# Kernel tuning notes

Measured on AMD Instinct MI355X. Metric: run time of the kernel, lower is better.

## Reference

```python
import jax, jax.numpy as jnp
import numpy as np

M_ANCH = 704   # 22 parts * 32 anchors
N_ANCH = 128   # object anchors


def reference(smpl_betas, object_rel_rotmat, object_rel_trans, object_anchors_org,
              v_template, shapedirs, J_regressor, pca_mean, pca_components,
              anchor_indices):
    b = smpl_betas.shape[0]
    v = v_template[None] + jnp.einsum('bk,vck->bvc', smpl_betas, shapedirs)   # [b,V,3]
    J = jnp.einsum('jv,bvc->bjc', J_regressor, v)                              # [b,55,3]
    v = v - J[:, :1]                                                           # root-center
    smpl_anchors = v[:, anchor_indices]                                        # [b,704,3]
    # --- encode: transform object anchors, broadcast offset diff, PCA ---
    obj_anchors = jnp.einsum('bnc,bdc->bnd', object_anchors_org, object_rel_rotmat) \
        + object_rel_trans[:, None, :]                                         # [b,128,3]
    offsets = obj_anchors[:, None, :, :] - smpl_anchors[:, :, None, :]         # [b,704,128,3]
    off_flat = offsets.reshape(b, -1)                                          # [b,270336]
    gamma = (off_flat - pca_mean[None]) @ pca_components.T                     # [b,128]
    # --- decode: PCA inverse ---
    off_rec = pca_mean[None] + gamma @ pca_components                          # [b,270336]
    # --- decode_object_RT: batched Procrustes via 3x3 SVD ---
    off4 = off_rec.reshape(b, M_ANCH, N_ANCH, 3)
    P = (smpl_anchors[:, :, None, :] + off4).reshape(b, -1, 3)                 # [b,m*n,3]
    Q = jnp.broadcast_to(object_anchors_org[:, None], (b, M_ANCH, N_ANCH, 3)).reshape(b, -1, 3)
    center_Q = Q.mean(axis=1, keepdims=True)
    Qc = Q - center_Q
    svd_mat = jnp.einsum('bic,bid->bcd', P, Qc)                                # P^T @ Qc, [b,3,3]
    u, s, vh = jnp.linalg.svd(svd_mat, full_matrices=False)
    d = jnp.linalg.det(u @ vh)                                                 # [b]
    dvec = jnp.concatenate([jnp.ones((b, 2), svd_mat.dtype), d[:, None]], axis=-1)
    R = (u * dvec[:, None, :]) @ vh                                            # u @ diag(1,1,d) @ vh
    T = (P - jnp.einsum('bij,bnj->bni', R, Q)).mean(axis=1)                    # [b,3]
    return gamma, R, T


def setup_inputs() -> dict:
    key = jax.random.key(0)
    ks = jax.random.split(key, 10)
    b, V, Jn, K = 64, 10475, 55, 10
    D = M_ANCH * N_ANCH * 3
    return {
        'smpl_betas': jax.random.normal(ks[0], (b, K), jnp.float32),
        'object_rel_rotmat': jax.random.normal(ks[1], (b, 3, 3), jnp.float32),
        'object_rel_trans': jax.random.normal(ks[2], (b, 3), jnp.float32),
        'object_anchors_org': jax.random.normal(ks[3], (b, N_ANCH, 3), jnp.float32),
        'v_template': jax.random.normal(ks[4], (V, 3), jnp.float32),
        'shapedirs': jax.random.normal(ks[5], (V, 3, K), jnp.float32) * 0.03,
        'J_regressor': jax.random.uniform(ks[6], (Jn, V), jnp.float32) / V,
        'pca_mean': jax.random.normal(ks[7], (D,), jnp.float32) * 0.1,
        'pca_components': jax.random.normal(ks[8], (128, D), jnp.float32) / np.sqrt(D),
        'anchor_indices': jax.random.randint(ks[9], (M_ANCH,), 0, V, jnp.int32),
    }
```

## Files before the change

### kernel.cpp

```cpp
#include <hip/hip_runtime.h>

#define V_CNT   10475
#define M_A     704
#define N_A     128
#define KB      10
#define D_TOT   270336
#define ROW384  384
#define NCHUNK  44
#define MT      16
#define LSTR    388

#define WS_JJ     0
#define WS_CMEAN  64
#define WS_MC     192
#define WS_V2C    576
#define WS_SASUM  960
#define WS_GWS    1152
#define WS_X      9344
#define WS_WP     169088
#define WS_UPART  488576
#define WS_TOTAL  2651264
#define WS_ZEROF  1152

#define NJ_BLK 28
#define NM_BLK 88
#define NP_BLK 64

__global__ __launch_bounds__(384) void k_pre(
    const float* __restrict__ Jr, const float* __restrict__ vt,
    const float* __restrict__ sd, const float* __restrict__ mean,
    const float* __restrict__ betas, const float* __restrict__ rot,
    const float* __restrict__ trans, const float* __restrict__ org,
    const int* __restrict__ anch,
    float* __restrict__ JJ, float* __restrict__ Mc,
    float* __restrict__ X, float* __restrict__ saSum) {
  __shared__ float orgL[384];
  __shared__ float red[384];
  __shared__ float small[24];
  const int blk = blockIdx.x, t = threadIdx.x;

  if (blk < NJ_BLK) {
    float acc[33];
#pragma unroll
    for (int i = 0; i < 33; ++i) acc[i] = 0.f;
    int v = blk * 384 + t;
    if (v < V_CNT) {
      float jr = Jr[v];
#pragma unroll
      for (int c = 0; c < 3; ++c) {
        acc[c] += jr * vt[v * 3 + c];
        const float* sp = sd + ((size_t)v * 3 + c) * KB;
#pragma unroll
        for (int k = 0; k < KB; ++k) acc[3 + c * KB + k] += jr * sp[k];
      }
    }
#pragma unroll
    for (int i = 0; i < 33; ++i) {
      float x = acc[i];
      for (int off = 32; off > 0; off >>= 1) x += __shfl_down(x, off);
      if ((t & 63) == 0) atomicAdd(&JJ[i], x);
    }
  } else if (blk < NJ_BLK + NM_BLK) {
    int j = blk - NJ_BLK;
    float a = 0.f;
#pragma unroll
    for (int mi = 0; mi < 8; ++mi)
      a += mean[(size_t)(j * 8 + mi) * ROW384 + t];
    atomicAdd(&Mc[t], a);
  } else {
    const int b = blk - (NJ_BLK + NM_BLK);
    if (t < 10) small[t] = betas[b * 10 + t];
    else if (t >= 10 && t < 19) small[t] = rot[b * 9 + (t - 10)];
    else if (t >= 19 && t < 22) small[t] = trans[b * 3 + (t - 19)];
    orgL[t] = org[(size_t)b * 384 + t];
    __syncthreads();
    {
      int n = t / 3, d = t % 3;
      X[(size_t)b * 2496 + t] =
          orgL[n * 3 + 0] * small[10 + d * 3 + 0] +
          orgL[n * 3 + 1] * small[10 + d * 3 + 1] +
          orgL[n * 3 + 2] * small[10 + d * 3 + 2] + small[19 + d];
    }
    float ps = 0.f;
    for (int e = t; e < 2112; e += 384) {
      int m = e / 3, c = e - m * 3;
      int a = anch[m];
      const float* sp = sd + ((size_t)a * 3 + c) * KB;
      float val = vt[a * 3 + c];
#pragma unroll
      for (int k = 0; k < KB; ++k) val += small[k] * sp[k];
      X[(size_t)b * 2496 + 384 + e] = val;
      ps += val;
    }
    red[t] = ps;
    __syncthreads();
    if (t < 3) {
      float s = 0.f;
#pragma unroll 8
      for (int j = 0; j < 128; ++j) s += red[t + 3 * j];
      saSum[b * 3 + t] = s;
    }
  }
}

__global__ __launch_bounds__(384) void k_pcpass(
    const float* __restrict__ pc, const float* __restrict__ mean,
    float* __restrict__ Upart, float* __restrict__ Wp,
    float* __restrict__ cmean) {
  __shared__ float tile[MT * LSTR];
  __shared__ float red[384];
  __shared__ float cred[6];
  const int t = threadIdx.x;
  const int pid = blockIdx.x & 127;
  const int chunk = blockIdx.x >> 7;
  const int m0 = chunk * MT;
  const float* row = pc + (size_t)pid * D_TOT + (size_t)m0 * ROW384;
  const float* mrow = mean + (size_t)m0 * ROW384;

  float cm = 0.f;
#pragma unroll
  for (int i = 0; i < 4; ++i) {
    int f = 1536 * i + 4 * t;
    float4 pv = *(const float4*)(row + f);
    float4 mv = *(const float4*)(mrow + f);
    cm += pv.x * mv.x + pv.y * mv.y + pv.z * mv.z + pv.w * mv.w;
    int m_l = 4 * i + t / 96;
    int col = (t % 96) * 4;
    *(float4*)(&tile[m_l * LSTR + col]) = pv;
  }
  __syncthreads();

  {
    float u = 0.f;
#pragma unroll
    for (int m = 0; m < MT; ++m) u += tile[m * LSTR + t];
    Upart[((size_t)chunk * 128 + pid) * 384 + t] = u;
  }
  {
    int grp = t / 48, mc = t % 48, m_l = mc / 3, c = mc % 3;
    const float* tp = &tile[m_l * LSTR + c];
    float vsp = 0.f;
#pragma unroll 8
    for (int j = 0; j < 16; ++j) vsp += tp[(grp * 16 + j) * 3];
    red[t] = vsp;
  }
  {
    float x = cm;
    for (int off = 32; off > 0; off >>= 1) x += __shfl_down(x, off);
    if ((t & 63) == 0) cred[t >> 6] = x;
  }
  __syncthreads();
  if (t < 48) {
    float vs = 0.f;
#pragma unroll
    for (int g = 0; g < 8; ++g) vs += red[g * 48 + t];
    Wp[(size_t)pid * 2496 + 384 + m0 * 3 + t] = -vs;
  }
  if (t == 0) {
    float s = cred[0] + cred[1] + cred[2] + cred[3] + cred[4] + cred[5];
    atomicAdd(&cmean[pid], s);
  }
}

__global__ __launch_bounds__(384) void k_red(
    const float* __restrict__ Upart, float* __restrict__ Wp,
    float* __restrict__ V2c) {
  __shared__ float red[384];
  const int pid = blockIdx.x, t = threadIdx.x;
  float u = 0.f;
#pragma unroll 4
  for (int c = 0; c < NCHUNK; ++c)
    u += Upart[((size_t)c * 128 + pid) * 384 + t];
  Wp[(size_t)pid * 2496 + t] = u;
  float s = 0.f;
  const float* vr = Wp + (size_t)pid * 2496 + 384;
#pragma unroll
  for (int j = 0; j < 6; ++j) {
    int idx = t + 384 * j;
    if (idx < 2112) s += vr[idx];
  }
  red[t] = s;
  __syncthreads();
  if (t < 3) {
    float acc = 0.f;
#pragma unroll 8
    for (int j = 0; j < 128; ++j) acc += red[t + 3 * j];
    V2c[t * 128 + pid] = -acc;
  }
}

__global__ __launch_bounds__(256) void k_gamma(
    const float* __restrict__ X, const float* __restrict__ Wp,
    float* __restrict__ gWS) {
  const int t = threadIdx.x;
  const int b = blockIdx.x >> 5, pg = blockIdx.x & 31;
  const int w = t >> 6, l = t & 63;
  const int p = pg * 4 + w;
  const float4* X4 = (const float4*)(X + (size_t)b * 2496);
  const float4* W4 = (const float4*)(Wp + (size_t)p * 2496);
  float s = 0.f;
#pragma unroll
  for (int i = 0; i < 10; ++i) {
    int idx = i * 64 + l;
    if (idx < 624) {
      float4 xv = X4[idx];
      float4 wv = W4[idx];
      s += xv.x * wv.x + xv.y * wv.y + xv.z * wv.z + xv.w * wv.w;
    }
  }
#pragma unroll
  for (int off = 32; off > 0; off >>= 1) s += __shfl_down(s, off);
  if (l == 0) gWS[b * 128 + p] = s;
}

__device__ inline double det3(const double A[3][3]) {
  return A[0][0] * (A[1][1] * A[2][2] - A[1][2] * A[2][1])
       - A[0][1] * (A[1][0] * A[2][2] - A[1][2] * A[2][0])
       + A[0][2] * (A[1][0] * A[2][1] - A[1][1] * A[2][0]);
}

__device__ void svd3_rotation(const float* S, float* Rout) {
  double M[3][3], B[3][3], Vv[3][3];
  for (int i = 0; i < 3; ++i)
    for (int j = 0; j < 3; ++j) M[i][j] = (double)S[i * 3 + j];
  for (int i = 0; i < 3; ++i)
    for (int j = 0; j < 3; ++j) {
      double a = 0;
      for (int k = 0; k < 3; ++k) a += M[k][i] * M[k][j];
      B[i][j] = a;
    }
  for (int i = 0; i < 3; ++i)
    for (int j = 0; j < 3; ++j) Vv[i][j] = (i == j) ? 1.0 : 0.0;
  const int PP[3] = {0, 0, 1}, QQ[3] = {1, 2, 2};
  for (int sweep = 0; sweep < 25; ++sweep) {
    double off = B[0][1] * B[0][1] + B[0][2] * B[0][2] + B[1][2] * B[1][2];
    double dg = B[0][0] * B[0][0] + B[1][1] * B[1][1] + B[2][2] * B[2][2];
    if (off <= 1e-28 * (dg + 1e-300)) break;
    for (int pr = 0; pr < 3; ++pr) {
      int p = PP[pr], q = QQ[pr];
      double apq = B[p][q];
      if (apq == 0.0) continue;
      double dd = (B[p][p] - B[q][q]) / (2.0 * apq);
      double tt = 1.0 / (fabs(dd) + sqrt(dd * dd + 1.0));
      if (dd < 0.0) tt = -tt;
      double cc = 1.0 / sqrt(tt * tt + 1.0), ss = tt * cc;
      B[p][p] += tt * apq;
      B[q][q] -= tt * apq;
      B[p][q] = B[q][p] = 0.0;
      int k = 3 - p - q;
      double Bkp = cc * B[k][p] + ss * B[k][q];
      double Bkq = -ss * B[k][p] + cc * B[k][q];
      B[k][p] = B[p][k] = Bkp;
      B[k][q] = B[q][k] = Bkq;
      for (int i = 0; i < 3; ++i) {
        double vip = cc * Vv[i][p] + ss * Vv[i][q];
        double viq = -ss * Vv[i][p] + cc * Vv[i][q];
        Vv[i][p] = vip;
        Vv[i][q] = viq;
      }
    }
  }
  double lam[3] = {B[0][0], B[1][1], B[2][2]};
  int o0 = 0, o1 = 1, o2 = 2, tp;
  if (lam[o0] < lam[o1]) { tp = o0; o0 = o1; o1 = tp; }
  if (lam[o0] < lam[o2]) { tp = o0; o0 = o2; o2 = tp; }
  if (lam[o1] < lam[o2]) { tp = o1; o1 = o2; o2 = tp; }
  int ord[3] = {o0, o1, o2};
  double sv[3], U[3][3], Vs[3][3];
  for (int j = 0; j < 3; ++j) {
    double l = lam[ord[j]];
    sv[j] = l > 0.0 ? sqrt(l) : 0.0;
    for (int i = 0; i < 3; ++i) Vs[i][j] = Vv[i][ord[j]];
  }
  for (int j = 0; j < 3; ++j) {
    double vx = Vs[0][j], vy = Vs[1][j], vz = Vs[2][j];
    double ux = M[0][0] * vx + M[0][1] * vy + M[0][2] * vz;
    double uy = M[1][0] * vx + M[1][1] * vy + M[1][2] * vz;
    double uz = M[2][0] * vx + M[2][1] * vy + M[2][2] * vz;
    double sj = sv[j];
    if (sj > 1e-12 * (sv[0] + 1e-300)) {
      U[0][j] = ux / sj; U[1][j] = uy / sj; U[2][j] = uz / sj;
    } else if (j == 2) {
      double cx = U[1][0] * U[2][1] - U[2][0] * U[1][1];
      double cy = U[2][0] * U[0][1] - U[0][0] * U[2][1];
      double cz = U[0][0] * U[1][1] - U[1][0] * U[0][1];
      double nn = sqrt(cx * cx + cy * cy + cz * cz);
      if (nn < 1e-300) { cx = 0; cy = 0; cz = 1; nn = 1; }
      U[0][2] = cx / nn; U[1][2] = cy / nn; U[2][2] = cz / nn;
    } else {
      U[0][j] = (j == 0) ? 1.0 : 0.0;
      U[1][j] = (j == 1) ? 1.0 : 0.0;
      U[2][j] = 0.0;
    }
  }
  double dsgn = (det3(U) * det3(Vs)) < 0.0 ? -1.0 : 1.0;
  for (int i = 0; i < 3; ++i)
    for (int j = 0; j < 3; ++j)
      Rout[i * 3 + j] = (float)(U[i][0] * Vs[j][0] + U[i][1] * Vs[j][1] +
                                dsgn * U[i][2] * Vs[j][2]);
}

__global__ __launch_bounds__(384) void k_finish(
    const float* __restrict__ betas, const float* __restrict__ org,
    const float* __restrict__ JJ, const float* __restrict__ cmean,
    const float* __restrict__ Mc, const float* __restrict__ V2c,
    const float* __restrict__ saSum, const float* __restrict__ gWS,
    const float* __restrict__ Wp, float* __restrict__ out) {
  const int b = blockIdx.x, t = threadIdx.x;
  __shared__ float orgL[384], A[384], gammaL[128];
  __shared__ float betasL[10], J0L[3], cQ[3], smat[9], RL[9];

  if (t < 10) betasL[t] = betas[b * 10 + t];
  orgL[t] = org[(size_t)b * 384 + t];
  __syncthreads();
  if (t < 3) {
    float j0 = JJ[t];
#pragma unroll
    for (int k = 0; k < KB; ++k) j0 += betasL[k] * JJ[3 + t * KB + k];
    J0L[t] = j0;
    float s = 0.f;
    for (int n = 0; n < N_A; ++n) s += orgL[n * 3 + t];
    cQ[t] = s * (1.f / 128.f);
  }
  __syncthreads();

  if (t < 128) {
    float g = gWS[b * 128 + t] + J0L[0] * V2c[t] + J0L[1] * V2c[128 + t] +
              J0L[2] * V2c[256 + t] - cmean[t];
    gammaL[t] = g;
    out[b * 128 + t] = g;
  }
  __syncthreads();

  {
    float gs = 0.f;
#pragma unroll 4
    for (int p = 0; p < 128; ++p) gs += gammaL[p] * Wp[(size_t)p * 2496 + t];
    A[t] = Mc[t] + gs;
  }
  __syncthreads();

  if (t < 9) {
    int c = t / 3, d = t % 3;
    float s = 0.f, cq = cQ[d];
    for (int n = 0; n < N_A; ++n) s += A[n * 3 + c] * (orgL[n * 3 + d] - cq);
    smat[t] = s;
  }
  __syncthreads();
  if (t == 0) svd3_rotation(smat, RL);
  __syncthreads();
  if (t < 9) out[8192 + b * 9 + t] = RL[t];
  if (t < 3) {
    float s2 = 0.f;
    for (int n = 0; n < N_A; ++n) s2 += A[n * 3 + t];
    float meanP = saSum[b * 3 + t] * (1.f / 704.f) - J0L[t] + s2 * (1.f / 90112.f);
    float rq = RL[t * 3 + 0] * cQ[0] + RL[t * 3 + 1] * cQ[1] + RL[t * 3 + 2] * cQ[2];
    out[8768 + b * 3 + t] = meanP - rq;
  }
}

extern "C" void kernel_launch(void* const* d_in, const int* in_sizes, int n_in,
                              void* d_out, int out_size, void* d_ws, size_t ws_size,
                              hipStream_t stream) {
  const float* betas = (const float*)d_in[0];
  const float* rot   = (const float*)d_in[1];
  const float* trans = (const float*)d_in[2];
  const float* org   = (const float*)d_in[3];
  const float* vt    = (const float*)d_in[4];
  const float* sd    = (const float*)d_in[5];
  const float* Jr    = (const float*)d_in[6];
  const float* mean  = (const float*)d_in[7];
  const float* pc    = (const float*)d_in[8];
  const int*   anch  = (const int*)d_in[9];
  float* out = (float*)d_out;
  float* ws  = (float*)d_ws;
  if (ws_size < (size_t)WS_TOTAL * sizeof(float)) return;

  float* JJ    = ws + WS_JJ;
  float* cmean = ws + WS_CMEAN;
  float* Mc    = ws + WS_MC;
  float* V2c   = ws + WS_V2C;
  float* saSum = ws + WS_SASUM;
  float* gWS   = ws + WS_GWS;
  float* X     = ws + WS_X;
  float* Wp    = ws + WS_WP;
  float* Upart = ws + WS_UPART;

  hipMemsetAsync(ws, 0, (size_t)WS_ZEROF * sizeof(float), stream);
  k_pre<<<NJ_BLK + NM_BLK + NP_BLK, 384, 0, stream>>>(
      Jr, vt, sd, mean, betas, rot, trans, org, anch, JJ, Mc, X, saSum);
  k_pcpass<<<NCHUNK * 128, 384, 0, stream>>>(pc, mean, Upart, Wp, cmean);
  k_red<<<128, 384, 0, stream>>>(Upart, Wp, V2c);
  k_gamma<<<64 * 32, 256, 0, stream>>>(X, Wp, gWS);
  k_finish<<<64, 384, 0, stream>>>(betas, org, JJ, cmean, Mc, V2c, saSum, gWS,
                                   Wp, out);
}
```

Baseline: 305.6 us.

## Replace global atomics with partial sums, split anchor gather, vectorize finish

```diff
diff --git a/kernel.cpp b/kernel.cpp
--- a/kernel.cpp
+++ b/kernel.cpp
@@ -10,21 +10,23 @@
 #define MT      16
 #define LSTR    388
 
-#define WS_JJ     0
-#define WS_CMEAN  64
-#define WS_MC     192
-#define WS_V2C    576
-#define WS_SASUM  960
-#define WS_GWS    1152
-#define WS_X      9344
-#define WS_WP     169088
-#define WS_UPART  488576
-#define WS_TOTAL  2651264
-#define WS_ZEROF  1152
+#define WS_JJP    0
+#define WS_JJ     960
+#define WS_MCP    1024
+#define WS_MC     34816
+#define WS_CMP    35200
+#define WS_CMEAN  40832
+#define WS_V2C    40960
+#define WS_SAP    41344
+#define WS_GWS    42112
+#define WS_X      50304
+#define WS_WP     210048
+#define WS_UPART  529536
+#define WS_TOTAL  2692224
 
 #define NJ_BLK 28
 #define NM_BLK 88
-#define NP_BLK 64
+#define NP_BLK 256
 
 __global__ __launch_bounds__(384) void k_pre(
     const float* __restrict__ Jr, const float* __restrict__ vt,
@@ -32,14 +34,17 @@
     const float* __restrict__ betas, const float* __restrict__ rot,
     const float* __restrict__ trans, const float* __restrict__ org,
     const int* __restrict__ anch,
-    float* __restrict__ JJ, float* __restrict__ Mc,
-    float* __restrict__ X, float* __restrict__ saSum) {
+    float* __restrict__ JJpart, float* __restrict__ Mcpart,
+    float* __restrict__ X, float* __restrict__ sapart) {
   __shared__ float orgL[384];
   __shared__ float red[384];
   __shared__ float small[24];
+  __shared__ float jjs[33];
   const int blk = blockIdx.x, t = threadIdx.x;
 
   if (blk < NJ_BLK) {
+    if (t < 33) jjs[t] = 0.f;
+    __syncthreads();
     float acc[33];
 #pragma unroll
     for (int i = 0; i < 33; ++i) acc[i] = 0.f;
@@ -58,23 +63,26 @@
     for (int i = 0; i < 33; ++i) {
       float x = acc[i];
       for (int off = 32; off > 0; off >>= 1) x += __shfl_down(x, off);
-      if ((t & 63) == 0) atomicAdd(&JJ[i], x);
-    }
+      if ((t & 63) == 0) atomicAdd(&jjs[i], x);
+    }
+    __syncthreads();
+    if (t < 33) JJpart[blk * 33 + t] = jjs[t];
   } else if (blk < NJ_BLK + NM_BLK) {
     int j = blk - NJ_BLK;
     float a = 0.f;
 #pragma unroll
     for (int mi = 0; mi < 8; ++mi)
       a += mean[(size_t)(j * 8 + mi) * ROW384 + t];
-    atomicAdd(&Mc[t], a);
+    Mcpart[(size_t)j * 384 + t] = a;
   } else {
-    const int b = blk - (NJ_BLK + NM_BLK);
+    const int idx = blk - (NJ_BLK + NM_BLK);
+    const int b = idx >> 2, sl = idx & 3;
     if (t < 10) small[t] = betas[b * 10 + t];
     else if (t >= 10 && t < 19) small[t] = rot[b * 9 + (t - 10)];
     else if (t >= 19 && t < 22) small[t] = trans[b * 3 + (t - 19)];
-    orgL[t] = org[(size_t)b * 384 + t];
+    if (sl == 0) orgL[t] = org[(size_t)b * 384 + t];
     __syncthreads();
-    {
+    if (sl == 0) {
       int n = t / 3, d = t % 3;
       X[(size_t)b * 2496 + t] =
           orgL[n * 3 + 0] * small[10 + d * 3 + 0] +
@@ -82,15 +90,20 @@
           orgL[n * 3 + 2] * small[10 + d * 3 + 2] + small[19 + d];
     }
     float ps = 0.f;
-    for (int e = t; e < 2112; e += 384) {
-      int m = e / 3, c = e - m * 3;
-      int a = anch[m];
-      const float* sp = sd + ((size_t)a * 3 + c) * KB;
-      float val = vt[a * 3 + c];
-#pragma unroll
-      for (int k = 0; k < KB; ++k) val += small[k] * sp[k];
-      X[(size_t)b * 2496 + 384 + e] = val;
-      ps += val;
+#pragma unroll
+    for (int r = 0; r < 2; ++r) {
+      int el = t + r * 384;
+      if (el < 528) {
+        int e = sl * 528 + el;
+        int m = e / 3, c = e - m * 3;
+        int a = anch[m];
+        const float* sp = sd + ((size_t)a * 3 + c) * KB;
+        float val = vt[a * 3 + c];
+#pragma unroll
+        for (int k = 0; k < KB; ++k) val += small[k] * sp[k];
+        X[(size_t)b * 2496 + 384 + e] = val;
+        ps += val;
+      }
     }
     red[t] = ps;
     __syncthreads();
@@ -98,7 +111,7 @@
       float s = 0.f;
 #pragma unroll 8
       for (int j = 0; j < 128; ++j) s += red[t + 3 * j];
-      saSum[b * 3 + t] = s;
+      sapart[idx * 3 + t] = s;
     }
   }
 }
@@ -106,7 +119,7 @@
 __global__ __launch_bounds__(384) void k_pcpass(
     const float* __restrict__ pc, const float* __restrict__ mean,
     float* __restrict__ Upart, float* __restrict__ Wp,
-    float* __restrict__ cmean) {
+    float* __restrict__ cmpart) {
   __shared__ float tile[MT * LSTR];
   __shared__ float red[384];
   __shared__ float cred[6];
@@ -156,17 +169,36 @@
     for (int g = 0; g < 8; ++g) vs += red[g * 48 + t];
     Wp[(size_t)pid * 2496 + 384 + m0 * 3 + t] = -vs;
   }
-  if (t == 0) {
-    float s = cred[0] + cred[1] + cred[2] + cred[3] + cred[4] + cred[5];
-    atomicAdd(&cmean[pid], s);
-  }
+  if (t == 0)
+    cmpart[chunk * 128 + pid] =
+        cred[0] + cred[1] + cred[2] + cred[3] + cred[4] + cred[5];
 }
 
 __global__ __launch_bounds__(384) void k_red(
-    const float* __restrict__ Upart, float* __restrict__ Wp,
-    float* __restrict__ V2c) {
+    const float* __restrict__ Upart, const float* __restrict__ JJpart,
+    const float* __restrict__ Mcpart, const float* __restrict__ cmpart,
+    float* __restrict__ Wp, float* __restrict__ V2c,
+    float* __restrict__ JJ, float* __restrict__ Mc,
+    float* __restrict__ cmean) {
+  const int t = threadIdx.x;
+  if (blockIdx.x == 128) {
+    if (t < 33) {
+      float s = 0.f;
+#pragma unroll 4
+      for (int j = 0; j < NJ_BLK; ++j) s += JJpart[j * 33 + t];
+      JJ[t] = s;
+    }
+    return;
+  }
+  if (blockIdx.x == 129) {
+    float s = 0.f;
+#pragma unroll 4
+    for (int j = 0; j < NM_BLK; ++j) s += Mcpart[(size_t)j * 384 + t];
+    Mc[t] = s;
+    return;
+  }
   __shared__ float red[384];
-  const int pid = blockIdx.x, t = threadIdx.x;
+  const int pid = blockIdx.x;
   float u = 0.f;
 #pragma unroll 4
   for (int c = 0; c < NCHUNK; ++c)
@@ -180,6 +212,12 @@
     if (idx < 2112) s += vr[idx];
   }
   red[t] = s;
+  if (t < 64) {
+    float x = (t < NCHUNK) ? cmpart[t * 128 + pid] : 0.f;
+#pragma unroll
+    for (int off = 32; off > 0; off >>= 1) x += __shfl_down(x, off);
+    if (t == 0) cmean[pid] = x;
+  }
   __syncthreads();
   if (t < 3) {
     float acc = 0.f;
@@ -304,10 +342,12 @@
     const float* __restrict__ betas, const float* __restrict__ org,
     const float* __restrict__ JJ, const float* __restrict__ cmean,
     const float* __restrict__ Mc, const float* __restrict__ V2c,
-    const float* __restrict__ saSum, const float* __restrict__ gWS,
+    const float* __restrict__ sapart, const float* __restrict__ gWS,
     const float* __restrict__ Wp, float* __restrict__ out) {
   const int b = blockIdx.x, t = threadIdx.x;
-  __shared__ float orgL[384], A[384], gammaL[128];
+  __shared__ float orgL[384];
+  __shared__ __align__(16) float A[384];
+  __shared__ float gammaL[128];
   __shared__ float betasL[10], J0L[3], cQ[3], smat[9], RL[9];
 
   if (t < 10) betasL[t] = betas[b * 10 + t];
@@ -332,11 +372,17 @@
   }
   __syncthreads();
 
-  {
-    float gs = 0.f;
+  if (t < 96) {
+    float4 gs = {0.f, 0.f, 0.f, 0.f};
 #pragma unroll 4
-    for (int p = 0; p < 128; ++p) gs += gammaL[p] * Wp[(size_t)p * 2496 + t];
-    A[t] = Mc[t] + gs;
+    for (int p = 0; p < 128; ++p) {
+      float4 w = *(const float4*)(Wp + (size_t)p * 2496 + 4 * t);
+      float g = gammaL[p];
+      gs.x += g * w.x; gs.y += g * w.y; gs.z += g * w.z; gs.w += g * w.w;
+    }
+    float4 m4 = *(const float4*)(Mc + 4 * t);
+    float4 a4 = {m4.x + gs.x, m4.y + gs.y, m4.z + gs.z, m4.w + gs.w};
+    *(float4*)(&A[4 * t]) = a4;
   }
   __syncthreads();
 
@@ -351,9 +397,11 @@
   __syncthreads();
   if (t < 9) out[8192 + b * 9 + t] = RL[t];
   if (t < 3) {
+    float sSum = sapart[(b * 4 + 0) * 3 + t] + sapart[(b * 4 + 1) * 3 + t] +
+                 sapart[(b * 4 + 2) * 3 + t] + sapart[(b * 4 + 3) * 3 + t];
     float s2 = 0.f;
     for (int n = 0; n < N_A; ++n) s2 += A[n * 3 + t];
-    float meanP = saSum[b * 3 + t] * (1.f / 704.f) - J0L[t] + s2 * (1.f / 90112.f);
+    float meanP = sSum * (1.f / 704.f) - J0L[t] + s2 * (1.f / 90112.f);
     float rq = RL[t * 3 + 0] * cQ[0] + RL[t * 3 + 1] * cQ[1] + RL[t * 3 + 2] * cQ[2];
     out[8768 + b * 3 + t] = meanP - rq;
   }
@@ -376,22 +424,25 @@
   float* ws  = (float*)d_ws;
   if (ws_size < (size_t)WS_TOTAL * sizeof(float)) return;
 
-  float* JJ    = ws + WS_JJ;
-  float* cmean = ws + WS_CMEAN;
-  float* Mc    = ws + WS_MC;
-  float* V2c   = ws + WS_V2C;
-  float* saSum = ws + WS_SASUM;
-  float* gWS   = ws + WS_GWS;
-  float* X     = ws + WS_X;
-  float* Wp    = ws + WS_WP;
-  float* Upart = ws + WS_UPART;
-
-  hipMemsetAsync(ws, 0, (size_t)WS_ZEROF * sizeof(float), stream);
+  float* JJpart = ws + WS_JJP;
+  float* JJ     = ws + WS_JJ;
+  float* Mcpart = ws + WS_MCP;
+  float* Mc     = ws + WS_MC;
+  float* cmpart = ws + WS_CMP;
+  float* cmean  = ws + WS_CMEAN;
+  float* V2c    = ws + WS_V2C;
+  float* sapart = ws + WS_SAP;
+  float* gWS    = ws + WS_GWS;
+  float* X      = ws + WS_X;
+  float* Wp     = ws + WS_WP;
+  float* Upart  = ws + WS_UPART;
+
   k_pre<<<NJ_BLK + NM_BLK + NP_BLK, 384, 0, stream>>>(
-      Jr, vt, sd, mean, betas, rot, trans, org, anch, JJ, Mc, X, saSum);
-  k_pcpass<<<NCHUNK * 128, 384, 0, stream>>>(pc, mean, Upart, Wp, cmean);
-  k_red<<<128, 384, 0, stream>>>(Upart, Wp, V2c);
+      Jr, vt, sd, mean, betas, rot, trans, org, anch, JJpart, Mcpart, X, sapart);
+  k_pcpass<<<NCHUNK * 128, 384, 0, stream>>>(pc, mean, Upart, Wp, cmpart);
+  k_red<<<130, 384, 0, stream>>>(Upart, JJpart, Mcpart, cmpart, Wp, V2c, JJ, Mc,
+                                 cmean);
   k_gamma<<<64 * 32, 256, 0, stream>>>(X, Wp, gWS);
-  k_finish<<<64, 384, 0, stream>>>(betas, org, JJ, cmean, Mc, V2c, saSum, gWS,
+  k_finish<<<64, 384, 0, stream>>>(betas, org, JJ, cmean, Mc, V2c, sapart, gWS,
                                    Wp, out);
 }
```

Measured after the change: 264.5 us. 1.16x faster.
